# Kernel tuning notes

Measured on AMD Instinct MI355X. Metric: run time of the kernel, lower is better.

## Reference

```python
import jax, jax.numpy as jnp
import numpy as np

B, S, D = 1, 4096, 2048
H, KVH, HD = 16, 4, 128  # heads, kv heads, head_dim
ROPE_BASE = 10000.0


def _rope_cos_sin(position_ids):
    # inv_freq: [HD/2]
    inv_freq = 1.0 / (ROPE_BASE ** (jnp.arange(0, HD, 2, dtype=jnp.float32) / HD))
    # freqs: [B, S, HD/2] -> emb: [B, S, HD] (concat(freqs, freqs))
    freqs = position_ids.astype(jnp.float32)[..., None] * inv_freq
    emb = jnp.concatenate([freqs, freqs], axis=-1)
    # [B, 1, S, HD] to broadcast over heads
    return jnp.cos(emb)[:, None, :, :], jnp.sin(emb)[:, None, :, :]


def _rotate_half(x):
    x1, x2 = x[..., : HD // 2], x[..., HD // 2 :]
    return jnp.concatenate([-x2, x1], axis=-1)


def setup_inputs() -> dict:
    key = jax.random.key(0)
    ks = jax.random.split(key, 5)
    s = 0.02
    return {
        "hidden_states": jax.random.normal(ks[0], (B, S, D), jnp.float32),
        "Wq": jax.random.normal(ks[1], (H * HD, D), jnp.float32) * s,
        "Wk": jax.random.normal(ks[2], (KVH * HD, D), jnp.float32) * s,
        "Wv": jax.random.normal(ks[3], (KVH * HD, D), jnp.float32) * s,
        "Wo": jax.random.normal(ks[4], (D, H * HD), jnp.float32) * s,
        "position_ids": jnp.arange(S, dtype=jnp.int64 if jax.config.jax_enable_x64 else jnp.int32)[None, :].repeat(B, 0),
    }


def reference(hidden_states, Wq, Wk, Wv, Wo, position_ids):
    b, s, _ = hidden_states.shape
    # projections (no bias): [b, s, nheads*hd] -> [b, nh, s, hd]
    q = (hidden_states @ Wq.T).reshape(b, s, H, HD).transpose(0, 2, 1, 3)
    k = (hidden_states @ Wk.T).reshape(b, s, KVH, HD).transpose(0, 2, 1, 3)
    v = (hidden_states @ Wv.T).reshape(b, s, KVH, HD).transpose(0, 2, 1, 3)

    cos, sin = _rope_cos_sin(position_ids)  # [b,1,s,hd]
    q = q * cos + _rotate_half(q) * sin
    k = k * cos + _rotate_half(k) * sin

    # GQA: repeat kv heads (repeat_interleave along head dim)
    n_rep = H // KVH
    k = jnp.repeat(k, n_rep, axis=1)
    v = jnp.repeat(v, n_rep, axis=1)

    # eager quadratic attention with causal mask
    scores = jnp.einsum("bhqd,bhkd->bhqk", q, k) / jnp.sqrt(jnp.float32(HD))
    causal = jnp.tril(jnp.ones((s, s), dtype=bool))
    scores = jnp.where(causal[None, None], scores, jnp.finfo(scores.dtype).min)
    attn = jax.nn.softmax(scores, axis=-1)
    out = jnp.einsum("bhqk,bhkd->bhqd", attn, v)  # [b,h,s,hd]
    out = out.transpose(0, 2, 1, 3).reshape(b, s, H * HD)
    return out @ Wo.T
```

## Files before the change

kernel.cpp:

```cpp
#include <hip/hip_runtime.h>
#include <hip/hip_bf16.h>

constexpr int S   = 4096;
constexpr int D   = 2048;
constexpr int H   = 16;
constexpr int KVH = 4;
constexpr int HD  = 128;

using short8 = __attribute__((ext_vector_type(8))) short;
using f32x4  = __attribute__((ext_vector_type(4))) float;
using f32x16 = __attribute__((ext_vector_type(16))) float;

__device__ inline ushort f2bf(float f) {
  union { float f; unsigned u; } x{f};
  unsigned r = x.u + 0x7FFFu + ((x.u >> 16) & 1u);
  return (ushort)(r >> 16);
}
__device__ inline float bf2f(ushort h) {
  union { unsigned u; float f; } x{(unsigned)h << 16};
  return x.f;
}
__device__ inline unsigned pkbf(float a, float b) {
  union { float f; unsigned u; } xa{a}, xb{b};
  unsigned ra = xa.u + 0x7FFFu + ((xa.u >> 16) & 1u);
  unsigned rb = xb.u + 0x7FFFu + ((xb.u >> 16) & 1u);
#if __has_builtin(__builtin_amdgcn_perm)
  return __builtin_amdgcn_perm(rb, ra, 0x07060302u);
#else
  return (rb & 0xFFFF0000u) | (ra >> 16);
#endif
}

__device__ inline void async_copy16(const ushort* g, ushort* l) {
  __builtin_amdgcn_global_load_lds(
      (const __attribute__((address_space(1))) unsigned int*)g,
      (__attribute__((address_space(3))) unsigned int*)l, 16, 0, 0);
}

constexpr size_t N_HID = (size_t)S * D;
constexpr size_t N_WQ  = (size_t)(H * HD) * D;
constexpr size_t N_WKV = (size_t)(KVH * HD) * D;
constexpr size_t C1_ = N_HID;
constexpr size_t C2_ = C1_ + N_WQ;
constexpr size_t C3_ = C2_ + N_WKV;
constexpr size_t C4_ = C3_ + N_WKV;
constexpr size_t C5_ = C4_ + N_WQ;

__global__ void cvt_all_kernel(const float* __restrict__ hid, const float* __restrict__ wq,
                               const float* __restrict__ wk, const float* __restrict__ wv,
                               const float* __restrict__ wo, ushort* __restrict__ dst) {
  size_t i = (size_t)blockIdx.x * blockDim.x + threadIdx.x;
  size_t off = i * 4;
  if (off >= C5_) return;
  const float* src;
  if      (off < C1_) src = hid + off;
  else if (off < C2_) src = wq + (off - C1_);
  else if (off < C3_) src = wk + (off - C2_);
  else if (off < C4_) src = wv + (off - C3_);
  else                src = wo + (off - C4_);
  float4 f = *(const float4*)src;
  ushort4 o;
  o.x = f2bf(f.x); o.y = f2bf(f.y); o.z = f2bf(f.z); o.w = f2bf(f.w);
  *(ushort4*)&dst[off] = o;
}

template <int OUT_MODE>
__device__ __forceinline__ void gemm_tile(const ushort* __restrict__ A,
                                          const ushort* __restrict__ Bt,
                                          void* __restrict__ Cv,
                                          int M, int N, int K, int bxi, int byi,
                                          ushort* As, ushort* Bs) {
  const int bm = byi * 128;
  const int bn = bxi * 128;
  const int tid  = threadIdx.x;
  const int lane = tid & 63;
  const int w    = tid >> 6;
  const int wr = w >> 1, wc = w & 1;
  const int lm = lane & 15, quad = lane >> 4;

  f32x4 acc[4][4];
#pragma unroll
  for (int i = 0; i < 4; ++i)
#pragma unroll
    for (int j = 0; j < 4; ++j) acc[i][j] = (f32x4){0.f, 0.f, 0.f, 0.f};

  for (int k0 = 0; k0 < K; k0 += 32) {
#pragma unroll
    for (int j = 0; j < 2; ++j) {
      int idx = j * 256 + tid;
      int row = idx >> 2;
      int col = (idx & 3) * 8;
      int ubase = (j * 256 + w * 64) * 8;
      async_copy16(A + (size_t)(bm + row) * K + k0 + col, &As[ubase]);
      async_copy16(Bt + (size_t)(bn + row) * K + k0 + col, &Bs[ubase]);
    }
    __syncthreads();
    short8 af[4], bfr[4];
#pragma unroll
    for (int t = 0; t < 4; ++t) {
      af[t]  = *(const short8*)&As[(wr * 64 + t * 16 + lm) * 32 + quad * 8];
      bfr[t] = *(const short8*)&Bs[(wc * 64 + t * 16 + lm) * 32 + quad * 8];
    }
#pragma unroll
    for (int i = 0; i < 4; ++i)
#pragma unroll
      for (int j = 0; j < 4; ++j)
        acc[i][j] = __builtin_amdgcn_mfma_f32_16x16x32_bf16(af[i], bfr[j], acc[i][j], 0, 0, 0);
    __syncthreads();
  }

#pragma unroll
  for (int i = 0; i < 4; ++i)
#pragma unroll
    for (int j = 0; j < 4; ++j) {
      if (OUT_MODE == 2) {
        int col  = bn + wc * 64 + j * 16 + lm;
        int rowb = bm + wr * 64 + i * 16 + quad * 4;
        ushort4 o4;
        o4.x = f2bf(acc[i][j][0]); o4.y = f2bf(acc[i][j][1]);
        o4.z = f2bf(acc[i][j][2]); o4.w = f2bf(acc[i][j][3]);
        *(ushort4*)&((ushort*)Cv)[(size_t)col * M + rowb] = o4;
      } else {
#pragma unroll
        for (int r = 0; r < 4; ++r) {
          size_t row = bm + wr * 64 + i * 16 + quad * 4 + r;
          size_t col = bn + wc * 64 + j * 16 + lm;
          if (OUT_MODE == 1) ((ushort*)Cv)[row * N + col] = f2bf(acc[i][j][r]);
          else               ((float*)Cv)[row * N + col]  = acc[i][j][r];
        }
      }
    }
}

__global__ __launch_bounds__(256) void gemm_qkv_kernel(const ushort* __restrict__ hb,
                                                       const ushort* __restrict__ wq,
                                                       const ushort* __restrict__ wk,
                                                       const ushort* __restrict__ wv,
                                                       ushort* __restrict__ qb,
                                                       ushort* __restrict__ kb,
                                                       ushort* __restrict__ vtb) {
  __shared__ __align__(16) ushort As[128 * 32];
  __shared__ __align__(16) ushort Bs[128 * 32];
  int bid = blockIdx.x;
  if (bid < 512) {
    gemm_tile<1>(hb, wq, qb, S, H * HD, D, bid & 15, bid >> 4, As, Bs);
  } else if (bid < 640) {
    int b = bid - 512;
    gemm_tile<1>(hb, wk, kb, S, KVH * HD, D, b & 3, b >> 2, As, Bs);
  } else {
    int b = bid - 640;
    gemm_tile<2>(hb, wv, vtb, S, KVH * HD, D, b & 3, b >> 2, As, Bs);
  }
}

template <int OUT_MODE>
__global__ __launch_bounds__(256) void gemm_bt_kernel(const ushort* __restrict__ A,
                                                      const ushort* __restrict__ Bt,
                                                      void* __restrict__ Cv,
                                                      int M, int N, int K) {
  __shared__ __align__(16) ushort As[128 * 32];
  __shared__ __align__(16) ushort Bs[128 * 32];
  gemm_tile<OUT_MODE>(A, Bt, Cv, M, N, K, blockIdx.x, blockIdx.y, As, Bs);
}

__global__ void rope_bf16_kernel(ushort* __restrict__ qb, ushort* __restrict__ kb,
                                 const int* __restrict__ pos_ids) {
  int idx = blockIdx.x * blockDim.x + threadIdx.x;
  const int total = S * (H + KVH) * (HD / 2);
  if (idx >= total) return;
  int j = idx & 63;
  int t = idx >> 6;
  int head = t % (H + KVH);
  int s = t / (H + KVH);
  float p = (float)pos_ids[s];
  float inv_freq = exp2f(-(float)j * (13.287712379549449f / 64.0f));
  float ang = p * inv_freq;
  float c = cosf(ang), sn = sinf(ang);
  ushort* base = (head < H) ? (qb + (size_t)s * (H * HD) + head * HD)
                            : (kb + (size_t)s * (KVH * HD) + (head - H) * HD);
  float x1 = bf2f(base[j]), x2 = bf2f(base[j + 64]);
  base[j]      = f2bf(x1 * c - x2 * sn);
  base[j + 64] = f2bf(x2 * c + x1 * sn);
}

__global__ __launch_bounds__(128, 2) void attn_mfma_kernel(const ushort* __restrict__ q,
                                                           const ushort* __restrict__ k,
                                                           const ushort* __restrict__ Vt,
                                                           ushort* __restrict__ o) {
  const int bid = blockIdx.x;
  const int h   = bid & 15;
  const int t   = bid >> 4;
  const int u   = t >> 4, sdx = t & 15;
  const int qi  = (u == 0) ? (63 - sdx) : (u == 1) ? (32 + sdx)
                : (u == 2) ? (31 - sdx) : sdx;
  const int q0  = qi * 64;
  const int kvh = h >> 2;
  const int tid  = threadIdx.x;
  const int lane = tid & 63;
  const int w    = tid >> 6;
  const int m32  = lane & 31;
  const int p    = lane >> 5;

  __shared__ __align__(16) ushort Kc[2][4096];
  __shared__ __align__(16) ushort Vs[2][4096];

  const int q0w = q0 + w * 32;

  short8 qf[8];
#pragma unroll
  for (int s = 0; s < 8; ++s)
    qf[s] = *(const short8*)&q[(size_t)(q0w + m32) * (H * HD) + h * HD + s * 16 + p * 8];

  f32x16 Oacc[4];
#pragma unroll
  for (int i = 0; i < 4; ++i)
#pragma unroll
    for (int r = 0; r < 16; ++r) Oacc[i][r] = 0.f;
  float lsum = 0.f;

  const int lr = lane >> 2, lc = (lane & 3) * 8;
  auto stage = [&](int k0, int buf) {
    if (w == 0) {
#pragma unroll
      for (int i = 0; i < 8; ++i) {
        int row  = (i & 1) * 16 + lr;
        int colh = (i >> 1) * 32 + lc;
        async_copy16(&k[(size_t)(k0 + row) * (KVH * HD) + kvh * HD + colh],
                     &Kc[buf][i * 512]);
      }
    } else {
#pragma unroll
      for (int i = 0; i < 8; ++i) {
        int vr = i * 16 + lr;
        async_copy16(&Vt[(size_t)(kvh * HD + vr) * S + k0 + lc],
                     &Vs[buf][i * 512]);
      }
    }
  };

  stage(0, 0);
  __syncthreads();

  const float C1  = 0.08838834764831845f * 1.4426950408889634f;
  const float F2n = -12.0f * 1.4426950408889634f;
  const int T = (q0 + 64) / 32;

  for (int tt = 0; tt < T; ++tt) {
    const int k0  = tt * 32;
    const int cur = tt & 1;
    if (tt + 1 < T) stage(k0 + 32, cur ^ 1);
    if (k0 <= q0w + 31) {
      const ushort* Kb = Kc[cur];
      const ushort* Vb = Vs[cur];

      f32x16 st;
#pragma unroll
      for (int r = 0; r < 16; ++r) st[r] = 0.f;
#pragma unroll
      for (int s = 0; s < 8; ++s) {
        short8 kf = *(const short8*)&Kb[(s >> 1) * 1024 + m32 * 32 + (s & 1) * 16 + p * 8];
        st = __builtin_amdgcn_mfma_f32_32x32x16_bf16(kf, qf[s], st, 0, 0, 0);
      }

      float pv[16];
      if (k0 == q0w) {
#pragma unroll
        for (int r = 0; r < 16; ++r) {
          int kvl = (r & 3) + 8 * (r >> 2) + 4 * p;
          float e = exp2f(fmaf(st[r], C1, F2n));
          e = (kvl > m32) ? 0.f : e;
          pv[r] = e; lsum += e;
        }
      } else {
#pragma unroll
        for (int r = 0; r < 16; ++r) {
          float e = exp2f(fmaf(st[r], C1, F2n));
          pv[r] = e; lsum += e;
        }
      }

      unsigned own2[4][2], oth[4][2];
#pragma unroll
      for (int g = 0; g < 4; ++g) {
        own2[g][0] = pkbf(pv[4 * g + 0], pv[4 * g + 1]);
        own2[g][1] = pkbf(pv[4 * g + 2], pv[4 * g + 3]);
        oth[g][0]  = __shfl_xor(own2[g][0], 32);
        oth[g][1]  = __shfl_xor(own2[g][1], 32);
      }
      short8 pf[2];
#pragma unroll
      for (int t2 = 0; t2 < 2; ++t2) {
        union { unsigned u4[4]; short8 s8; } pb;
        pb.u4[0] = p ? oth[2 * t2 + 1][0] : own2[2 * t2][0];
        pb.u4[1] = p ? oth[2 * t2 + 1][1] : own2[2 * t2][1];
        pb.u4[2] = p ? own2[2 * t2 + 1][0] : oth[2 * t2][0];
        pb.u4[3] = p ? own2[2 * t2 + 1][1] : oth[2 * t2][1];
        pf[t2] = pb.s8;
      }

#pragma unroll
      for (int ht = 0; ht < 4; ++ht)
#pragma unroll
        for (int t2 = 0; t2 < 2; ++t2) {
          short8 vf = *(const short8*)&Vb[ht * 1024 + m32 * 32 + t2 * 16 + p * 8];
          Oacc[ht] = __builtin_amdgcn_mfma_f32_32x32x16_bf16(vf, pf[t2], Oacc[ht], 0, 0, 0);
        }
    }
    __syncthreads();
  }

  float ltot = lsum + __shfl_xor(lsum, 32);
  float inv = 1.0f / ltot;
#pragma unroll
  for (int ht = 0; ht < 4; ++ht)
#pragma unroll
    for (int rq = 0; rq < 4; ++rq) {
      uint2 dd;
      dd.x = pkbf(Oacc[ht][4 * rq + 0] * inv, Oacc[ht][4 * rq + 1] * inv);
      dd.y = pkbf(Oacc[ht][4 * rq + 2] * inv, Oacc[ht][4 * rq + 3] * inv);
      *(uint2*)&o[(size_t)(q0w + m32) * (H * HD) + h * HD + ht * 32 + 8 * rq + 4 * p] = dd;
    }
}

extern "C" void kernel_launch(void* const* d_in, const int* in_sizes, int n_in,
                              void* d_out, int out_size, void* d_ws, size_t ws_size,
                              hipStream_t stream) {
  const float* hidden = (const float*)d_in[0];
  const float* Wq     = (const float*)d_in[1];
  const float* Wk     = (const float*)d_in[2];
  const float* Wv     = (const float*)d_in[3];
  const float* Wo     = (const float*)d_in[4];
  const int*   pos    = (const int*)d_in[5];
  float* out = (float*)d_out;

  ushort* hb  = (ushort*)d_ws;
  ushort* wqb = hb  + N_HID;
  ushort* wkb = wqb + N_WQ;
  ushort* wvb = wkb + N_WKV;
  ushort* wob = wvb + N_WKV;
  ushort* qb  = wob + N_WQ;
  ushort* kb  = qb  + (size_t)S * (H * HD);
  ushort* vtb = kb  + (size_t)S * (KVH * HD);
  ushort* ob  = vtb + (size_t)(KVH * HD) * S;

  dim3 blk(256);
  size_t n4 = C5_ / 4;
  cvt_all_kernel<<<(int)((n4 + 255) / 256), blk, 0, stream>>>(hidden, Wq, Wk, Wv, Wo, hb);

  gemm_qkv_kernel<<<dim3(768), blk, 0, stream>>>(hb, wqb, wkb, wvb, qb, kb, vtb);

  int rope_total = S * (H + KVH) * (HD / 2);
  rope_bf16_kernel<<<(rope_total + 255) / 256, blk, 0, stream>>>(qb, kb, pos);

  attn_mfma_kernel<<<dim3(1024), dim3(128), 0, stream>>>(qb, kb, vtb, ob);

  gemm_bt_kernel<0><<<dim3(D / 128, S / 128), blk, 0, stream>>>(ob, wob, out, S, D, D);
}
```

Measured before the change: 390.9 us.

## Enlarge attention tiles to 128 queries and 64 keys with 4-wave blocks

```diff
diff --git a/kernel.cpp b/kernel.cpp
--- a/kernel.cpp
+++ b/kernel.cpp
@@ -28,6 +28,21 @@
   return __builtin_amdgcn_perm(rb, ra, 0x07060302u);
 #else
   return (rb & 0xFFFF0000u) | (ra >> 16);
+#endif
+}
+__device__ inline unsigned pkbf_t(float a, float b) {
+  union { float f; unsigned u; } xa{a}, xb{b};
+#if __has_builtin(__builtin_amdgcn_perm)
+  return __builtin_amdgcn_perm(xb.u, xa.u, 0x07060302u);
+#else
+  return (xb.u & 0xFFFF0000u) | (xa.u >> 16);
+#endif
+}
+__device__ inline float fast_exp2(float x) {
+#if __has_builtin(__builtin_amdgcn_exp2f)
+  return __builtin_amdgcn_exp2f(x);
+#else
+  return exp2f(x);
 #endif
 }
 
@@ -183,17 +198,16 @@
   base[j + 64] = f2bf(x2 * c + x1 * sn);
 }
 
-__global__ __launch_bounds__(128, 2) void attn_mfma_kernel(const ushort* __restrict__ q,
+__global__ __launch_bounds__(256, 2) void attn_mfma_kernel(const ushort* __restrict__ q,
                                                            const ushort* __restrict__ k,
                                                            const ushort* __restrict__ Vt,
                                                            ushort* __restrict__ o) {
   const int bid = blockIdx.x;
   const int h   = bid & 15;
   const int t   = bid >> 4;
-  const int u   = t >> 4, sdx = t & 15;
-  const int qi  = (u == 0) ? (63 - sdx) : (u == 1) ? (32 + sdx)
-                : (u == 2) ? (31 - sdx) : sdx;
-  const int q0  = qi * 64;
+  const int tl  = t & 15, hi = t >> 4;
+  const int qi  = hi ? (2 * tl) : (31 - 2 * tl);
+  const int q0  = qi * 128;
   const int kvh = h >> 2;
   const int tid  = threadIdx.x;
   const int lane = tid & 63;
@@ -201,8 +215,8 @@
   const int m32  = lane & 31;
   const int p    = lane >> 5;
 
-  __shared__ __align__(16) ushort Kc[2][4096];
-  __shared__ __align__(16) ushort Vs[2][4096];
+  __shared__ __align__(16) ushort Kc[2][8192];
+  __shared__ __align__(16) ushort Vs[2][8192];
 
   const int q0w = q0 + w * 32;
 
@@ -218,22 +232,19 @@
     for (int r = 0; r < 16; ++r) Oacc[i][r] = 0.f;
   float lsum = 0.f;
 
-  const int lr = lane >> 2, lc = (lane & 3) * 8;
   auto stage = [&](int k0, int buf) {
-    if (w == 0) {
-#pragma unroll
-      for (int i = 0; i < 8; ++i) {
-        int row  = (i & 1) * 16 + lr;
-        int colh = (i >> 1) * 32 + lc;
-        async_copy16(&k[(size_t)(k0 + row) * (KVH * HD) + kvh * HD + colh],
-                     &Kc[buf][i * 512]);
-      }
-    } else {
-#pragma unroll
-      for (int i = 0; i < 8; ++i) {
-        int vr = i * 16 + lr;
-        async_copy16(&Vt[(size_t)(kvh * HD + vr) * S + k0 + lc],
-                     &Vs[buf][i * 512]);
+#pragma unroll
+    for (int i = 0; i < 8; ++i) {
+      int c = w * 8 + i;
+      if (c < 16) {
+        int kh = c >> 3, s = c & 7;
+        async_copy16(&k[(size_t)(k0 + kh * 32 + m32) * (KVH * HD) + kvh * HD + s * 16 + p * 8],
+                     &Kc[buf][c * 512]);
+      } else {
+        int cv = c - 16;
+        int ht = cv >> 2, t2 = cv & 3;
+        async_copy16(&Vt[(size_t)(kvh * HD + ht * 32 + m32) * S + k0 + t2 * 16 + p * 8],
+                     &Vs[buf][cv * 512]);
       }
     }
   };
@@ -243,68 +254,75 @@
 
   const float C1  = 0.08838834764831845f * 1.4426950408889634f;
   const float F2n = -12.0f * 1.4426950408889634f;
-  const int T = (q0 + 64) / 32;
+  const int T = 2 * qi + 2;
 
   for (int tt = 0; tt < T; ++tt) {
-    const int k0  = tt * 32;
+    const int k0  = tt * 64;
     const int cur = tt & 1;
-    if (tt + 1 < T) stage(k0 + 32, cur ^ 1);
-    if (k0 <= q0w + 31) {
-      const ushort* Kb = Kc[cur];
-      const ushort* Vb = Vs[cur];
-
-      f32x16 st;
-#pragma unroll
-      for (int r = 0; r < 16; ++r) st[r] = 0.f;
-#pragma unroll
-      for (int s = 0; s < 8; ++s) {
-        short8 kf = *(const short8*)&Kb[(s >> 1) * 1024 + m32 * 32 + (s & 1) * 16 + p * 8];
-        st = __builtin_amdgcn_mfma_f32_32x32x16_bf16(kf, qf[s], st, 0, 0, 0);
+    if (tt + 1 < T) stage(k0 + 64, cur ^ 1);
+    const ushort* Kb = Kc[cur];
+    const ushort* Vb = Vs[cur];
+
+#pragma unroll
+    for (int kh = 0; kh < 2; ++kh) {
+      const int kbase = k0 + kh * 32;
+      if (kbase <= q0w + 31) {
+        f32x16 stA, stB;
+#pragma unroll
+        for (int r = 0; r < 16; ++r) { stA[r] = 0.f; stB[r] = 0.f; }
+#pragma unroll
+        for (int s = 0; s < 8; s += 2) {
+          short8 kf0 = *(const short8*)&Kb[(kh * 8 + s) * 512 + lane * 8];
+          short8 kf1 = *(const short8*)&Kb[(kh * 8 + s + 1) * 512 + lane * 8];
+          stA = __builtin_amdgcn_mfma_f32_32x32x16_bf16(kf0, qf[s], stA, 0, 0, 0);
+          stB = __builtin_amdgcn_mfma_f32_32x32x16_bf16(kf1, qf[s + 1], stB, 0, 0, 0);
+        }
+
+        float pv[16];
+        if (kbase == q0w) {
+#pragma unroll
+          for (int r = 0; r < 16; ++r) {
+            int kvl = (r & 3) + 8 * (r >> 2) + 4 * p;
+            float e = fast_exp2(fmaf(stA[r] + stB[r], C1, F2n));
+            e = (kvl > m32) ? 0.f : e;
+            pv[r] = e; lsum += e;
+          }
+        } else {
+#pragma unroll
+          for (int r = 0; r < 16; ++r) {
+            float e = fast_exp2(fmaf(stA[r] + stB[r], C1, F2n));
+            pv[r] = e; lsum += e;
+          }
+        }
+
+        unsigned own2[4][2], oth[4][2];
+#pragma unroll
+        for (int g = 0; g < 4; ++g) {
+          own2[g][0] = pkbf_t(pv[4 * g + 0], pv[4 * g + 1]);
+          own2[g][1] = pkbf_t(pv[4 * g + 2], pv[4 * g + 3]);
+          oth[g][0]  = __shfl_xor(own2[g][0], 32);
+          oth[g][1]  = __shfl_xor(own2[g][1], 32);
+        }
+        short8 pf[2];
+#pragma unroll
+        for (int t2 = 0; t2 < 2; ++t2) {
+          union { unsigned u4[4]; short8 s8; } pb;
+          pb.u4[0] = p ? oth[2 * t2 + 1][0] : own2[2 * t2][0];
+          pb.u4[1] = p ? oth[2 * t2 + 1][1] : own2[2 * t2][1];
+          pb.u4[2] = p ? own2[2 * t2 + 1][0] : oth[2 * t2][0];
+          pb.u4[3] = p ? own2[2 * t2 + 1][1] : oth[2 * t2][1];
+          pf[t2] = pb.s8;
+        }
+
+#pragma unroll
+        for (int ht = 0; ht < 4; ++ht)
+#pragma unroll
+          for (int t2l = 0; t2l < 2; ++t2l) {
+            int cv = ht * 4 + kh * 2 + t2l;
+            short8 vf = *(const short8*)&Vb[cv * 512 + lane * 8];
+            Oacc[ht] = __builtin_amdgcn_mfma_f32_32x32x16_bf16(vf, pf[t2l], Oacc[ht], 0, 0, 0);
+          }
       }
-
-      float pv[16];
-      if (k0 == q0w) {
-#pragma unroll
-        for (int r = 0; r < 16; ++r) {
-          int kvl = (r & 3) + 8 * (r >> 2) + 4 * p;
-          float e = exp2f(fmaf(st[r], C1, F2n));
-          e = (kvl > m32) ? 0.f : e;
-          pv[r] = e; lsum += e;
-        }
-      } else {
-#pragma unroll
-        for (int r = 0; r < 16; ++r) {
-          float e = exp2f(fmaf(st[r], C1, F2n));
-          pv[r] = e; lsum += e;
-        }
-      }
-
-      unsigned own2[4][2], oth[4][2];
-#pragma unroll
-      for (int g = 0; g < 4; ++g) {
-        own2[g][0] = pkbf(pv[4 * g + 0], pv[4 * g + 1]);
-        own2[g][1] = pkbf(pv[4 * g + 2], pv[4 * g + 3]);
-        oth[g][0]  = __shfl_xor(own2[g][0], 32);
-        oth[g][1]  = __shfl_xor(own2[g][1], 32);
-      }
-      short8 pf[2];
-#pragma unroll
-      for (int t2 = 0; t2 < 2; ++t2) {
-        union { unsigned u4[4]; short8 s8; } pb;
-        pb.u4[0] = p ? oth[2 * t2 + 1][0] : own2[2 * t2][0];
-        pb.u4[1] = p ? oth[2 * t2 + 1][1] : own2[2 * t2][1];
-        pb.u4[2] = p ? own2[2 * t2 + 1][0] : oth[2 * t2][0];
-        pb.u4[3] = p ? own2[2 * t2 + 1][1] : oth[2 * t2][1];
-        pf[t2] = pb.s8;
-      }
-
-#pragma unroll
-      for (int ht = 0; ht < 4; ++ht)
-#pragma unroll
-        for (int t2 = 0; t2 < 2; ++t2) {
-          short8 vf = *(const short8*)&Vb[ht * 1024 + m32 * 32 + t2 * 16 + p * 8];
-          Oacc[ht] = __builtin_amdgcn_mfma_f32_32x32x16_bf16(vf, pf[t2], Oacc[ht], 0, 0, 0);
-        }
     }
     __syncthreads();
   }
@@ -352,7 +370,7 @@
   int rope_total = S * (H + KVH) * (HD / 2);
   rope_bf16_kernel<<<(rope_total + 255) / 256, blk, 0, stream>>>(qb, kb, pos);
 
-  attn_mfma_kernel<<<dim3(1024), dim3(128), 0, stream>>>(qb, kb, vtb, ob);
+  attn_mfma_kernel<<<dim3(512), blk, 0, stream>>>(qb, kb, vtb, ob);
 
   gemm_bt_kernel<0><<<dim3(D / 128, S / 128), blk, 0, stream>>>(ob, wob, out, S, D, D);
 }
```

Measured after the change: 355.0 us. 9.2% less time.
